# Performance work log

Measured on AMD Instinct MI355X. Metric: run time of the kernel, lower is better.

## Reference

```python
import jax, jax.numpy as jnp
import numpy as np


def setup_inputs() -> dict:
    key = jax.random.key(0)
    k1, k2, k3, k4, k5 = jax.random.split(key, 5)
    B, C, H, W = 8, 512, 64, 64
    mid = C // 8
    x = jax.random.normal(k1, (B, C, H, W), dtype=jnp.float32)
    # 1x1 convs (no bias) are just channel-mixing matrices
    Wb = jax.random.normal(k2, (mid, C), dtype=jnp.float32) * (1.0 / np.sqrt(C))
    Wc = jax.random.normal(k3, (mid, C), dtype=jnp.float32) * (1.0 / np.sqrt(C))
    Wd = jax.random.normal(k4, (C, C), dtype=jnp.float32) * (1.0 / np.sqrt(C))
    gamma = jax.random.normal(k5, (1,), dtype=jnp.float32)
    return {"x": x, "Wb": Wb, "Wc": Wc, "Wd": Wd, "gamma": gamma}


def reference(x, Wb, Wc, Wd, gamma):
    B, C, H, W = x.shape
    N = H * W
    xf = x.reshape(B, C, N)                          # (B, C, N)
    b = jnp.einsum('mc,bcn->bnm', Wb, xf)            # queries  (B, N, mid)
    c = jnp.einsum('mc,bcn->bmn', Wc, xf)            # keys     (B, mid, N)
    d = jnp.einsum('oc,bcn->bno', Wd, xf)            # values   (B, N, C)
    # unscaled scores, softmax over keys (last dim), as in the source
    attn = jax.nn.softmax(jnp.einsum('bnm,bmk->bnk', b, c), axis=-1)  # (B, N, N)
    out = jnp.einsum('bnk,bko->bno', attn, d)        # (B, N, C)
    out = out.transpose(0, 2, 1).reshape(B, C, H, W)
    return gamma * out + x
```

## Files before the change

kernel.cpp:

```cpp
#include <hip/hip_runtime.h>

typedef unsigned short u16;
typedef _Float16 f16x8 __attribute__((ext_vector_type(8)));
typedef short bf16x8 __attribute__((ext_vector_type(8)));
typedef float f32x16 __attribute__((ext_vector_type(16)));
typedef unsigned int u32x4 __attribute__((ext_vector_type(4)));
typedef unsigned int u32x2 __attribute__((ext_vector_type(2)));

#define LOG2E 1.44269504088896340736f

static __device__ __forceinline__ u16 f2h(float f){
  union { _Float16 h; u16 u; } v; v.h = (_Float16)f; return v.u;
}
static __device__ __forceinline__ u16 f2bf(float f){
  union { float f; unsigned u; } v; v.f = f;
  return (u16)((v.u + 0x7fffu + ((v.u >> 16) & 1u)) >> 16);
}
static __device__ __forceinline__ unsigned pk2bf(float lo, float hi){
  unsigned r; asm("v_cvt_pk_bf16_f32 %0, %1, %2" : "=v"(r) : "v"(lo), "v"(hi)); return r;
}
static __device__ __forceinline__ float ex2(float x){
#if __has_builtin(__builtin_amdgcn_exp2f)
  return __builtin_amdgcn_exp2f(x);
#else
  return exp2f(x);
#endif
}
#define PSWAP(a, b) asm("v_permlane32_swap_b32 %0, %1" : "+v"(a), "+v"(b))

__global__ __launch_bounds__(256) void k_wcvt(const float* __restrict__ wb, const float* __restrict__ wc,
                                              const float* __restrict__ wd, u16* __restrict__ w16){
  int row = blockIdx.x, t = threadIdx.x;
  const float* src; float sc;
  if (row < 512)      { src = wd + (size_t)row * 512;        sc = 1.0f;  }
  else if (row < 576) { src = wb + (size_t)(row - 512) * 512; sc = LOG2E; }
  else                { src = wc + (size_t)(row - 576) * 512; sc = 1.0f;  }
  float2 v = *(const float2*)(src + t * 2);
  unsigned pk = (unsigned)f2h(v.x * sc) | ((unsigned)f2h(v.y * sc) << 16);
  *(unsigned*)(w16 + (size_t)row * 512 + t * 2) = pk;
}

__global__ __launch_bounds__(512, 1) void k_fused(const float* __restrict__ x, const u16* __restrict__ w16,
                                                  u16* __restrict__ qkb, u16* __restrict__ vtb){
  __shared__ u16 ltmp[64 * 140];
  __shared__ u16 lx[128 * 68];
  __shared__ u16 lw[640 * 68];
  int bx = blockIdx.x;
  int b = bx >> 5, nb = bx & 31;
  int t = threadIdx.x, w = t >> 6, l = t & 63, hi = l >> 5, ln = l & 31;
  int i = w & 1, j = w >> 1;
  size_t b4096 = (size_t)b * 4096;
  f32x16 acc[5][2] = {};
  int cS = t >> 3, ncS = t & 7;
  int nT = t & 127, q4 = t >> 7;
  const float* xbase = x + ((size_t)(b * 512 + cS)) * 4096 + nb * 128 + ncS * 16;
  float4 xpre[4];
#pragma unroll
  for (int g = 0; g < 4; ++g) xpre[g] = *(const float4*)(xbase + g * 4);
  for (int kt = 0; kt < 8; ++kt) {
    int c0 = kt * 64;
    {
      u16* d = &ltmp[cS * 140 + ncS * 16];
#pragma unroll
      for (int g = 0; g < 4; ++g) {
        float4 v = xpre[g];
        unsigned lo = (unsigned)f2h(v.x) | ((unsigned)f2h(v.y) << 16);
        unsigned h2 = (unsigned)f2h(v.z) | ((unsigned)f2h(v.w) << 16);
        *(u32x2*)(d + g * 4) = u32x2{lo, h2};
      }
    }
#pragma unroll
    for (int k10 = 0; k10 < 10; ++k10) {
      int slot = t + 512 * k10;
      int row = slot >> 3, ch8 = slot & 7;
      u32x4 wv = *(const u32x4*)(w16 + (size_t)row * 512 + c0 + ch8 * 8);
      u16* d = &lw[row * 68 + ch8 * 8];
      *(u32x2*)d       = u32x2{wv[0], wv[1]};
      *(u32x2*)(d + 4) = u32x2{wv[2], wv[3]};
    }
    __syncthreads();
    if (kt < 7) {
      const float* xp = xbase + (size_t)(kt + 1) * 64 * 4096;
#pragma unroll
      for (int g = 0; g < 4; ++g) xpre[g] = *(const float4*)(xp + g * 4);
    }
    {
      u16 tmp[16];
#pragma unroll
      for (int k = 0; k < 16; ++k) tmp[k] = ltmp[(q4 * 16 + k) * 140 + nT];
      u16* d = &lx[nT * 68 + q4 * 16];
#pragma unroll
      for (int g = 0; g < 4; ++g) {
        unsigned lo = (unsigned)tmp[g * 4]     | ((unsigned)tmp[g * 4 + 1] << 16);
        unsigned h2 = (unsigned)tmp[g * 4 + 2] | ((unsigned)tmp[g * 4 + 3] << 16);
        *(u32x2*)(d + g * 4) = u32x2{lo, h2};
      }
    }
    __syncthreads();
#pragma unroll
    for (int cc = 0; cc < 4; ++cc) {
      union { u32x2 d[2]; f16x8 v; } bf[2];
#pragma unroll
      for (int u = 0; u < 2; ++u) {
        const u16* p = &lx[(i * 64 + u * 32 + ln) * 68 + cc * 16 + hi * 8];
        bf[u].d[0] = *(const u32x2*)p; bf[u].d[1] = *(const u32x2*)(p + 4);
      }
#pragma unroll
      for (int s = 0; s < 5; ++s) {
        union { u32x2 d[2]; f16x8 v; } af;
        const u16* p = &lw[(j * 160 + s * 32 + ln) * 68 + cc * 16 + hi * 8];
        af.d[0] = *(const u32x2*)p; af.d[1] = *(const u32x2*)(p + 4);
#pragma unroll
        for (int u = 0; u < 2; ++u)
          acc[s][u] = __builtin_amdgcn_mfma_f32_32x32x16_f16(af.v, bf[u].v, acc[s][u], 0, 0, 0);
      }
    }
    __syncthreads();
  }
#pragma unroll
  for (int s = 0; s < 5; ++s) {
    int rt = j * 160 + s * 32;
    if (rt < 512) {
#pragma unroll
      for (int u = 0; u < 2; ++u) {
        int n = nb * 128 + i * 64 + u * 32 + ln;
#pragma unroll
        for (int r = 0; r < 16; ++r) {
          int o = rt + (r & 3) + 8 * (r >> 2) + 4 * hi;
          vtb[((size_t)(b * 512 + o)) * 4096 + n] = f2bf(acc[s][u][r]);
        }
      }
    }
  }
  u16* qkl = lw;
  if (j == 3) {
#pragma unroll
    for (int s = 1; s < 5; ++s) {
      int mbase = (s - 1) * 32;
#pragma unroll
      for (int u = 0; u < 2; ++u) {
        int nl = i * 64 + u * 32 + ln;
#pragma unroll
        for (int r = 0; r < 16; ++r) {
          int m = mbase + (r & 3) + 8 * (r >> 2) + 4 * hi;
          qkl[nl * 132 + m] = f2h(acc[s][u][r]);
        }
      }
    }
  }
  __syncthreads();
  {
    int n2 = t >> 2, ch = t & 3;
    u16* dst = qkb + (b4096 + nb * 128 + n2) * 128 + ch * 32;
#pragma unroll
    for (int g = 0; g < 4; ++g) {
      u32x2 d0 = *(const u32x2*)(&qkl[n2 * 132 + ch * 32 + g * 8]);
      u32x2 d1 = *(const u32x2*)(&qkl[n2 * 132 + ch * 32 + g * 8 + 4]);
      *(u32x4*)(dst + g * 8) = u32x4{d0[0], d0[1], d1[0], d1[1]};
    }
  }
}

__global__ __launch_bounds__(512, 1) void k_attn2(const u16* __restrict__ qk, const u16* __restrict__ vt,
                                                  const float* __restrict__ x, const float* __restrict__ gamma,
                                                  float* __restrict__ out){
  __shared__ char smem[87040];
  int bx = blockIdx.x;
  int orig = (bx & 7) * 32 + (bx >> 3);
  int combo = orig >> 4, qt = orig & 15;
  int b = combo >> 1, oc2 = combo & 1;
  int obase = oc2 * 256;
  int t = threadIdx.x, w = t >> 6, l = t & 63, hi = l >> 5, ln = l & 31;
  int q = qt * 256 + w * 32 + ln;
  size_t b4096 = (size_t)b * 4096;
  f16x8 qf[4];
  {
    const u16* qrow = qk + (b4096 + q) * 128;
#pragma unroll
    for (int ch = 0; ch < 4; ++ch) qf[ch] = *(const f16x8*)(qrow + ch * 16 + hi * 8);
  }
  int rowS = t >> 3, chS = t & 7;
  unsigned w8 = (unsigned)(rowS * 17 + chS * 2);
  unsigned rb8[4];
#pragma unroll
  for (int cc = 0; cc < 4; ++cc)
    rb8[cc] = (unsigned)(ln * 17 + cc * 4 + hi * 2);
  const u16* gK = qk + (b4096 + rowS) * 128 + 64 + chS * 8;
  const u16* gV0 = vt + ((size_t)(b * 512 + obase + rowS)) * 4096 + chS * 8;
  const u16* gV1 = gV0 + (size_t)64 * 4096;
  const u16* gV2 = gV0 + (size_t)128 * 4096;
  const u16* gV3 = gV0 + (size_t)192 * 4096;
  u32x4 kreg = *(const u32x4*)gK;
  u32x4 vr0 = *(const u32x4*)gV0, vr1 = *(const u32x4*)gV1;
  u32x4 vr2 = *(const u32x4*)gV2, vr3 = *(const u32x4*)gV3;
  {
    char* bp = smem;
    *(u32x2*)(bp + w8 * 8)              = u32x2{kreg[0], kreg[1]};
    *(u32x2*)(bp + w8 * 8 + 8)          = u32x2{kreg[2], kreg[3]};
    *(u32x2*)(bp + 8704  + w8 * 8)      = u32x2{vr0[0], vr0[1]};
    *(u32x2*)(bp + 8704  + w8 * 8 + 8)  = u32x2{vr0[2], vr0[3]};
    *(u32x2*)(bp + 17408 + w8 * 8)      = u32x2{vr1[0], vr1[1]};
    *(u32x2*)(bp + 17408 + w8 * 8 + 8)  = u32x2{vr1[2], vr1[3]};
    *(u32x2*)(bp + 26112 + w8 * 8)      = u32x2{vr2[0], vr2[1]};
    *(u32x2*)(bp + 26112 + w8 * 8 + 8)  = u32x2{vr2[2], vr2[3]};
    *(u32x2*)(bp + 34816 + w8 * 8)      = u32x2{vr3[0], vr3[1]};
    *(u32x2*)(bp + 34816 + w8 * 8 + 8)  = u32x2{vr3[2], vr3[3]};
  }
  gK += 8192; gV0 += 64; gV1 += 64; gV2 += 64; gV3 += 64;
  f32x16 acc[8] = {};
  float lacc = 0.0f;
  for (int kt = 0; kt < 64; ++kt) {
    __syncthreads();
    char* bufp = smem + (kt & 1) * 43520;
    char* bufn = smem + ((kt + 1) & 1) * 43520;
    if (kt < 63) {
      kreg = *(const u32x4*)gK;
      vr0 = *(const u32x4*)gV0; vr1 = *(const u32x4*)gV1;
      vr2 = *(const u32x4*)gV2; vr3 = *(const u32x4*)gV3;
      gK += 8192; gV0 += 64; gV1 += 64; gV2 += 64; gV3 += 64;
    }
    f32x16 s0 = {}, s1 = {};
    __builtin_amdgcn_s_setprio(1);
#pragma unroll
    for (int cc = 0; cc < 4; ++cc) {
      union { u32x2 d[2]; f16x8 v; } k0, k1;
      const char* p0 = bufp + rb8[cc] * 8;
      const char* p1 = p0 + 4352;
      k0.d[0] = *(const u32x2*)p0;  k0.d[1] = *(const u32x2*)(p0 + 8);
      k1.d[0] = *(const u32x2*)p1;  k1.d[1] = *(const u32x2*)(p1 + 8);
      s0 = __builtin_amdgcn_mfma_f32_32x32x16_f16(k0.v, qf[cc], s0, 0, 0, 0);
      s1 = __builtin_amdgcn_mfma_f32_32x32x16_f16(k1.v, qf[cc], s1, 0, 0, 0);
    }
    __builtin_amdgcn_s_setprio(0);
#pragma unroll
    for (int r = 0; r < 16; ++r) s0[r] = ex2(s0[r]);
#pragma unroll
    for (int r = 0; r < 16; ++r) s1[r] = ex2(s1[r]);
    {
      float p[16];
#pragma unroll
      for (int r = 0; r < 16; ++r) p[r] = s0[r] + s1[r];
#pragma unroll
      for (int d = 8; d >= 1; d >>= 1)
#pragma unroll
        for (int r = 0; r < d; ++r) p[r] += p[r + d];
      lacc += p[0];
    }
    unsigned c0[8], c1[8];
#pragma unroll
    for (int ii = 0; ii < 8; ++ii) c0[ii] = pk2bf(s0[2 * ii], s0[2 * ii + 1]);
#pragma unroll
    for (int ii = 0; ii < 8; ++ii) c1[ii] = pk2bf(s1[2 * ii], s1[2 * ii + 1]);
    PSWAP(c0[0], c0[2]); PSWAP(c0[1], c0[3]); PSWAP(c0[4], c0[6]); PSWAP(c0[5], c0[7]);
    PSWAP(c1[0], c1[2]); PSWAP(c1[1], c1[3]); PSWAP(c1[4], c1[6]); PSWAP(c1[5], c1[7]);
    union U8 { unsigned u[4]; bf16x8 v; } pa[4];
#pragma unroll
    for (int jj = 0; jj < 4; ++jj) { pa[0].u[jj] = c0[jj]; pa[1].u[jj] = c0[4 + jj]; pa[2].u[jj] = c1[jj]; pa[3].u[jj] = c1[4 + jj]; }
    __builtin_amdgcn_s_setprio(1);
#pragma unroll
    for (int kc = 0; kc < 4; ++kc) {
      const char* pv = bufp + 8704 + rb8[kc] * 8;
#pragma unroll
      for (int ot = 0; ot < 8; ++ot) {
        union { u32x2 d[2]; bf16x8 v; } vb;
        const char* p = pv + ot * 4352;
        vb.d[0] = *(const u32x2*)p;  vb.d[1] = *(const u32x2*)(p + 8);
        acc[ot] = __builtin_amdgcn_mfma_f32_32x32x16_bf16(pa[kc].v, vb.v, acc[ot], 0, 0, 0);
      }
    }
    __builtin_amdgcn_s_setprio(0);
    if (kt < 63) {
      *(u32x2*)(bufn + w8 * 8)              = u32x2{kreg[0], kreg[1]};
      *(u32x2*)(bufn + w8 * 8 + 8)          = u32x2{kreg[2], kreg[3]};
      *(u32x2*)(bufn + 8704  + w8 * 8)      = u32x2{vr0[0], vr0[1]};
      *(u32x2*)(bufn + 8704  + w8 * 8 + 8)  = u32x2{vr0[2], vr0[3]};
      *(u32x2*)(bufn + 17408 + w8 * 8)      = u32x2{vr1[0], vr1[1]};
      *(u32x2*)(bufn + 17408 + w8 * 8 + 8)  = u32x2{vr1[2], vr1[3]};
      *(u32x2*)(bufn + 26112 + w8 * 8)      = u32x2{vr2[0], vr2[1]};
      *(u32x2*)(bufn + 26112 + w8 * 8 + 8)  = u32x2{vr2[2], vr2[3]};
      *(u32x2*)(bufn + 34816 + w8 * 8)      = u32x2{vr3[0], vr3[1]};
      *(u32x2*)(bufn + 34816 + w8 * 8 + 8)  = u32x2{vr3[2], vr3[3]};
    }
  }
  float l_tot = lacc + __shfl_xor(lacc, 32);
  float sinv = gamma[0] / l_tot;
  __syncthreads();
  float* tb = (float*)smem + w * 1056;
#pragma unroll
  for (int ot = 0; ot < 8; ++ot) {
#pragma unroll
    for (int r = 0; r < 16; ++r) {
      int qr = (r & 3) + 8 * (r >> 2) + 4 * hi;
      tb[ln * 33 + qr] = acc[ot][r];
    }
#pragma unroll
    for (int it = 0; it < 16; ++it) {
      int orow = it * 2 + hi;
      float v = tb[orow * 33 + ln];
      size_t gi = (((size_t)(b * 512 + obase + ot * 32 + orow)) << 12) + (size_t)(qt * 256 + w * 32 + ln);
      out[gi] = sinv * v + x[gi];
    }
    __syncthreads();
  }
}

extern "C" void kernel_launch(void* const* d_in, const int* in_sizes, int n_in,
                              void* d_out, int out_size, void* d_ws, size_t ws_size,
                              hipStream_t stream) {
  (void)in_sizes; (void)n_in; (void)out_size; (void)ws_size;
  const float* x     = (const float*)d_in[0];
  const float* wb    = (const float*)d_in[1];
  const float* wc    = (const float*)d_in[2];
  const float* wd    = (const float*)d_in[3];
  const float* gamma = (const float*)d_in[4];
  float* out = (float*)d_out;
  char* ws = (char*)d_ws;
  u16* w16 = (u16*)ws;
  u16* qkb = (u16*)(ws + 1048576);
  u16* vtb = (u16*)(ws + 9437184);
  k_wcvt <<<dim3(640), dim3(256), 0, stream>>>(wb, wc, wd, w16);
  k_fused<<<dim3(256), dim3(512), 0, stream>>>(x, w16, qkb, vtb);
  k_attn2<<<dim3(256), dim3(512), 0, stream>>>(qkb, vtb, x, gamma, out);
}
```

Baseline: 223.6 us.

## Stream K/V tiles with direct global-to-LDS loads and XOR-swizzled layout

Replaces the register-staged K and V tile loads (global to VGPR, then paired 8-byte LDS writes into a padded layout) with global_load_lds DMA that writes 16-byte chunks straight into LDS. Bank conflicts are now avoided by an XOR swizzle on the global column, so the padding goes away and the MFMA operands become single 16-byte LDS reads. This removes VGPR pressure and the LDS store instructions from the inner loop. The risk is that correctness now depends on the async LDS writes being visible at the next __syncthreads and on the swizzled read addresses matching the write layout.

```diff
diff --git a/kernel.cpp b/kernel.cpp
--- a/kernel.cpp
+++ b/kernel.cpp
@@ -27,6 +27,10 @@
 #endif
 }
 #define PSWAP(a, b) asm("v_permlane32_swap_b32 %0, %1" : "+v"(a), "+v"(b))
+
+typedef __attribute__((address_space(3))) unsigned int lds_u32;
+typedef __attribute__((address_space(1))) const unsigned int glob_u32;
+#define GLL(gp, lp) __builtin_amdgcn_global_load_lds((glob_u32*)(gp), (lds_u32*)(lp), 16, 0, 0)
 
 __global__ __launch_bounds__(256) void k_wcvt(const float* __restrict__ wb, const float* __restrict__ wc,
                                               const float* __restrict__ wd, u16* __restrict__ w16){
@@ -164,7 +168,7 @@
 __global__ __launch_bounds__(512, 1) void k_attn2(const u16* __restrict__ qk, const u16* __restrict__ vt,
                                                   const float* __restrict__ x, const float* __restrict__ gamma,
                                                   float* __restrict__ out){
-  __shared__ char smem[87040];
+  __shared__ char smem[81920];
   int bx = blockIdx.x;
   int orig = (bx & 7) * 32 + (bx >> 3);
   int combo = orig >> 4, qt = orig & 15;
@@ -179,57 +183,43 @@
 #pragma unroll
     for (int ch = 0; ch < 4; ++ch) qf[ch] = *(const f16x8*)(qrow + ch * 16 + hi * 8);
   }
-  int rowS = t >> 3, chS = t & 7;
-  unsigned w8 = (unsigned)(rowS * 17 + chS * 2);
-  unsigned rb8[4];
+  unsigned rb[4];
 #pragma unroll
   for (int cc = 0; cc < 4; ++cc)
-    rb8[cc] = (unsigned)(ln * 17 + cc * 4 + hi * 2);
-  const u16* gK = qk + (b4096 + rowS) * 128 + 64 + chS * 8;
-  const u16* gV0 = vt + ((size_t)(b * 512 + obase + rowS)) * 4096 + chS * 8;
-  const u16* gV1 = gV0 + (size_t)64 * 4096;
-  const u16* gV2 = gV0 + (size_t)128 * 4096;
-  const u16* gV3 = gV0 + (size_t)192 * 4096;
-  u32x4 kreg = *(const u32x4*)gK;
-  u32x4 vr0 = *(const u32x4*)gV0, vr1 = *(const u32x4*)gV1;
-  u32x4 vr2 = *(const u32x4*)gV2, vr3 = *(const u32x4*)gV3;
-  {
-    char* bp = smem;
-    *(u32x2*)(bp + w8 * 8)              = u32x2{kreg[0], kreg[1]};
-    *(u32x2*)(bp + w8 * 8 + 8)          = u32x2{kreg[2], kreg[3]};
-    *(u32x2*)(bp + 8704  + w8 * 8)      = u32x2{vr0[0], vr0[1]};
-    *(u32x2*)(bp + 8704  + w8 * 8 + 8)  = u32x2{vr0[2], vr0[3]};
-    *(u32x2*)(bp + 17408 + w8 * 8)      = u32x2{vr1[0], vr1[1]};
-    *(u32x2*)(bp + 17408 + w8 * 8 + 8)  = u32x2{vr1[2], vr1[3]};
-    *(u32x2*)(bp + 26112 + w8 * 8)      = u32x2{vr2[0], vr2[1]};
-    *(u32x2*)(bp + 26112 + w8 * 8 + 8)  = u32x2{vr2[2], vr2[3]};
-    *(u32x2*)(bp + 34816 + w8 * 8)      = u32x2{vr3[0], vr3[1]};
-    *(u32x2*)(bp + 34816 + w8 * 8 + 8)  = u32x2{vr3[2], vr3[3]};
-  }
-  gK += 8192; gV0 += 64; gV1 += 64; gV2 += 64; gV3 += 64;
+    rb[cc] = (unsigned)(ln * 128 + (((cc << 5) | (hi << 4)) ^ ((ln & 7) << 4)));
+  int row = t >> 3;
+  int ch2 = ((t & 7) ^ (row & 7)) * 8;
+  const u16* gK = qk + (b4096 + row) * 128 + 64 + ch2;
+  const u16* gV = vt + ((size_t)(b * 512 + obase + row)) * 4096 + ch2;
+  unsigned ldsW = (unsigned)(w * 1024);
+  GLL(gK,            smem + ldsW);
+  GLL(gV,            smem + 8192  + ldsW);
+  GLL(gV + 262144,   smem + 16384 + ldsW);
+  GLL(gV + 524288,   smem + 24576 + ldsW);
+  GLL(gV + 786432,   smem + 32768 + ldsW);
+  gK += 8192; gV += 64;
   f32x16 acc[8] = {};
   float lacc = 0.0f;
   for (int kt = 0; kt < 64; ++kt) {
     __syncthreads();
-    char* bufp = smem + (kt & 1) * 43520;
-    char* bufn = smem + ((kt + 1) & 1) * 43520;
+    char* bufp = smem + (kt & 1) * 40960;
     if (kt < 63) {
-      kreg = *(const u32x4*)gK;
-      vr0 = *(const u32x4*)gV0; vr1 = *(const u32x4*)gV1;
-      vr2 = *(const u32x4*)gV2; vr3 = *(const u32x4*)gV3;
-      gK += 8192; gV0 += 64; gV1 += 64; gV2 += 64; gV3 += 64;
+      char* bufn = smem + ((kt + 1) & 1) * 40960;
+      GLL(gK,            bufn + ldsW);
+      GLL(gV,            bufn + 8192  + ldsW);
+      GLL(gV + 262144,   bufn + 16384 + ldsW);
+      GLL(gV + 524288,   bufn + 24576 + ldsW);
+      GLL(gV + 786432,   bufn + 32768 + ldsW);
+      gK += 8192; gV += 64;
     }
     f32x16 s0 = {}, s1 = {};
     __builtin_amdgcn_s_setprio(1);
 #pragma unroll
     for (int cc = 0; cc < 4; ++cc) {
-      union { u32x2 d[2]; f16x8 v; } k0, k1;
-      const char* p0 = bufp + rb8[cc] * 8;
-      const char* p1 = p0 + 4352;
-      k0.d[0] = *(const u32x2*)p0;  k0.d[1] = *(const u32x2*)(p0 + 8);
-      k1.d[0] = *(const u32x2*)p1;  k1.d[1] = *(const u32x2*)(p1 + 8);
-      s0 = __builtin_amdgcn_mfma_f32_32x32x16_f16(k0.v, qf[cc], s0, 0, 0, 0);
-      s1 = __builtin_amdgcn_mfma_f32_32x32x16_f16(k1.v, qf[cc], s1, 0, 0, 0);
+      f16x8 k0 = *(const f16x8*)(bufp + rb[cc]);
+      f16x8 k1 = *(const f16x8*)(bufp + 4096 + rb[cc]);
+      s0 = __builtin_amdgcn_mfma_f32_32x32x16_f16(k0, qf[cc], s0, 0, 0, 0);
+      s1 = __builtin_amdgcn_mfma_f32_32x32x16_f16(k1, qf[cc], s1, 0, 0, 0);
     }
     __builtin_amdgcn_s_setprio(0);
 #pragma unroll
@@ -259,28 +249,14 @@
     __builtin_amdgcn_s_setprio(1);
 #pragma unroll
     for (int kc = 0; kc < 4; ++kc) {
-      const char* pv = bufp + 8704 + rb8[kc] * 8;
+      const char* pv = bufp + 8192 + rb[kc];
 #pragma unroll
       for (int ot = 0; ot < 8; ++ot) {
-        union { u32x2 d[2]; bf16x8 v; } vb;
-        const char* p = pv + ot * 4352;
-        vb.d[0] = *(const u32x2*)p;  vb.d[1] = *(const u32x2*)(p + 8);
-        acc[ot] = __builtin_amdgcn_mfma_f32_32x32x16_bf16(pa[kc].v, vb.v, acc[ot], 0, 0, 0);
+        bf16x8 vb = *(const bf16x8*)(pv + ot * 4096);
+        acc[ot] = __builtin_amdgcn_mfma_f32_32x32x16_bf16(pa[kc].v, vb, acc[ot], 0, 0, 0);
       }
     }
     __builtin_amdgcn_s_setprio(0);
-    if (kt < 63) {
-      *(u32x2*)(bufn + w8 * 8)              = u32x2{kreg[0], kreg[1]};
-      *(u32x2*)(bufn + w8 * 8 + 8)          = u32x2{kreg[2], kreg[3]};
-      *(u32x2*)(bufn + 8704  + w8 * 8)      = u32x2{vr0[0], vr0[1]};
-      *(u32x2*)(bufn + 8704  + w8 * 8 + 8)  = u32x2{vr0[2], vr0[3]};
-      *(u32x2*)(bufn + 17408 + w8 * 8)      = u32x2{vr1[0], vr1[1]};
-      *(u32x2*)(bufn + 17408 + w8 * 8 + 8)  = u32x2{vr1[2], vr1[3]};
-      *(u32x2*)(bufn + 26112 + w8 * 8)      = u32x2{vr2[0], vr2[1]};
-      *(u32x2*)(bufn + 26112 + w8 * 8 + 8)  = u32x2{vr2[2], vr2[3]};
-      *(u32x2*)(bufn + 34816 + w8 * 8)      = u32x2{vr3[0], vr3[1]};
-      *(u32x2*)(bufn + 34816 + w8 * 8 + 8)  = u32x2{vr3[2], vr3[3]};
-    }
   }
   float l_tot = lacc + __shfl_xor(lacc, 32);
   float sinv = gamma[0] / l_tot;
```

After: 218.3 us, median of 2. 2.4% less time.
